# Kernel tuning notes

Hardware: AMD Instinct MI355X
Metric: run time of the kernel (lower is better)

The kernel has to match this reference:

```python
import jax, jax.numpy as jnp
import numpy as np
import math

N_EMBD = 2048
N_HEAD = 16
HEAD_DIM = N_EMBD // N_HEAD
B, T = 2, 2048


def setup_inputs() -> dict:
    key = jax.random.key(0)
    k1, k2, k3 = jax.random.split(key, 3)
    x = jax.random.normal(k1, (B, T, N_EMBD), dtype=jnp.float32)
    # Linear weights stored torch-style [out, in]; applied as x @ W.T
    W_gate = jax.random.normal(k2, (N_HEAD, N_EMBD), dtype=jnp.float32) * 0.02
    W_qkv = jax.random.normal(k3, (3 * N_EMBD, N_EMBD), dtype=jnp.float32) * 0.02
    return {"x": x, "W_gate": W_gate, "W_qkv": W_qkv}


def reference(x, W_gate, W_qkv):
    Bb, Tt, C = x.shape
    H, hd = N_HEAD, HEAD_DIM
    # --- top-1 head gating ---
    gating = jax.nn.softmax(x @ W_gate.T, axis=-1)            # [B,T,H]
    idx = jnp.argmax(gating, axis=-1)                          # [B,T]
    indicator = jax.nn.one_hot(idx, H, dtype=gating.dtype)     # [B,T,H] (no grad, like scatter of ones)
    top1_val = jnp.max(gating, axis=-1, keepdims=True)         # [B,T,1]
    gating_top1 = indicator * top1_val                         # [B,T,H]
    # --- qkv projection ---
    qkv = x @ W_qkv.T                                          # [B,T,3C]
    q, k, v = jnp.split(qkv, 3, axis=-1)
    k = k.reshape(Bb, Tt, H, hd)
    v = v.reshape(Bb, Tt, H, hd)
    # scatter-style weighted collapse of heads -> single shared K/V head (MQA)
    k_shared = jnp.einsum('bth,bthd->btd', indicator, k)       # [B,T,hd]
    v_shared = jnp.einsum('bth,bthd->btd', gating_top1, v)     # [B,T,hd]
    q = q.reshape(Bb, Tt, H, hd).transpose(0, 2, 1, 3)         # [B,H,T,hd]
    # --- causal softmax attention (materialized, as in source) ---
    att = jnp.einsum('bhqd,bkd->bhqk', q, k_shared) * (1.0 / math.sqrt(hd))
    causal = jnp.tril(jnp.ones((Tt, Tt), dtype=bool))          # [T,T]
    att = jnp.where(causal[None, None, :, :], att, -jnp.inf)
    att = jax.nn.softmax(att, axis=-1)
    y = jnp.einsum('bhqk,bkd->bhqd', att, v_shared)            # [B,H,T,hd]
    y = y.transpose(0, 2, 1, 3).reshape(Bb, Tt, C)
    return y
```

## Files before the change

### kernel.cpp

```cpp
#include <hip/hip_runtime.h>
#include <math.h>
#include <cstddef>

#define BB 2
#define TT 2048
#define CC 2048
#define HH 16
#define HD 128
#define MM (BB * TT)
#define QKV_N 6144
#define BK 32

typedef __attribute__((ext_vector_type(8))) short short8;
typedef __attribute__((ext_vector_type(4))) float f32x4;

__device__ __forceinline__ unsigned short f2bf(float f) {
    union { float f; unsigned int u; } v; v.f = f;
    unsigned int r = v.u + 0x7FFFu + ((v.u >> 16) & 1u);
    return (unsigned short)(r >> 16);
}
__device__ __forceinline__ unsigned short f2bf_up(float f) {
    union { float f; unsigned int u; } v; v.f = f;
    return (unsigned short)((v.u + 0x8000u) >> 16);
}
__device__ __forceinline__ float bf2f(unsigned short s) {
    union { unsigned int u; float f; } v; v.u = ((unsigned int)s) << 16;
    return v.f;
}
__device__ __forceinline__ void gload16(const void* g, void* l) {
    __builtin_amdgcn_global_load_lds(
        (const __attribute__((address_space(1))) unsigned int*)g,
        (__attribute__((address_space(3))) unsigned int*)l, 16, 0, 0);
}

__global__ __launch_bounds__(256) void gate_kernel(const float* __restrict__ x,
                                                   const float* __restrict__ Wg,
                                                   int* __restrict__ idxbuf,
                                                   float* __restrict__ top1buf,
                                                   unsigned short* __restrict__ xb) {
    int m = blockIdx.x;
    int tid = threadIdx.x;
    int h = tid >> 4;
    int j = tid & 15;
    const float4* xr = (const float4*)(x + (size_t)m * CC);
    const float4* wr = (const float4*)(Wg + (size_t)h * CC);
    float acc = 0.f;
#pragma unroll 8
    for (int i = 0; i < CC / 4; i += 16) {
        float4 a = xr[i + j];
        float4 b = wr[i + j];
        acc += a.x * b.x + a.y * b.y + a.z * b.z + a.w * b.w;
    }
    for (int off = 8; off > 0; off >>= 1) acc += __shfl_down(acc, off, 16);
    __shared__ float logits[HH];
    if (j == 0) logits[h] = acc;
    {
        float4 a = xr[tid * 2], b = xr[tid * 2 + 1];
        union { unsigned short s[8]; uint4 u; } pk;
        pk.s[0] = f2bf(a.x); pk.s[1] = f2bf(a.y); pk.s[2] = f2bf(a.z); pk.s[3] = f2bf(a.w);
        pk.s[4] = f2bf(b.x); pk.s[5] = f2bf(b.y); pk.s[6] = f2bf(b.z); pk.s[7] = f2bf(b.w);
        ((uint4*)(xb + (size_t)m * CC))[tid] = pk.u;
    }
    __syncthreads();
    if (tid == 0) {
        float zmax = logits[0];
        int best = 0;
        for (int i = 1; i < HH; i++) {
            if (logits[i] > zmax) { zmax = logits[i]; best = i; }
        }
        float s = 0.f;
        for (int i = 0; i < HH; i++) s += expf(logits[i] - zmax);
        idxbuf[m] = best;
        top1buf[m] = 1.0f / s;
    }
}

__global__ __launch_bounds__(256) void convert_bf16(const float* __restrict__ src,
                                                    unsigned short* __restrict__ dst,
                                                    int n8) {
    int i = blockIdx.x * 256 + threadIdx.x;
    if (i >= n8) return;
    const float4* s4 = (const float4*)src;
    float4 a = s4[i * 2], b = s4[i * 2 + 1];
    union { unsigned short s[8]; uint4 u; } pk;
    pk.s[0] = f2bf(a.x); pk.s[1] = f2bf(a.y); pk.s[2] = f2bf(a.z); pk.s[3] = f2bf(a.w);
    pk.s[4] = f2bf(b.x); pk.s[5] = f2bf(b.y); pk.s[6] = f2bf(b.z); pk.s[7] = f2bf(b.w);
    ((uint4*)dst)[i] = pk.u;
}

__global__ __launch_bounds__(256) void qproj_gemm(const unsigned short* __restrict__ A,
                                                  const unsigned short* __restrict__ Bm,
                                                  unsigned short* __restrict__ C) {
    __shared__ unsigned short As[2][128 * BK];
    __shared__ unsigned short Bs[2][128 * BK];
    int tid = threadIdx.x;
    int wave = tid >> 6, lane = tid & 63;
    int l = lane & 15, g = lane >> 4;
    int m0 = blockIdx.y * 128, n0 = blockIdx.x * 128;
    int wr = wave >> 1, wc = wave & 1;

    f32x4 acc[4][4];
#pragma unroll
    for (int i = 0; i < 4; i++)
#pragma unroll
        for (int j = 0; j < 4; j++) acc[i][j] = (f32x4){0.f, 0.f, 0.f, 0.f};

    int srow = lane >> 2;
    int scol = (lane & 3) * 8;
    const unsigned short* aB0 = A + (size_t)(m0 + wave * 32 + srow) * 2048 + scol;
    const unsigned short* bB0 = Bm + (size_t)(n0 + wave * 32 + srow) * 2048 + scol;

#define QSTAGE(k0_, bi) do {                                                   \
        gload16(aB0 + (k0_), &As[bi][wave * 1024]);                            \
        gload16(aB0 + (k0_) + (size_t)16 * 2048, &As[bi][wave * 1024 + 512]);  \
        gload16(bB0 + (k0_), &Bs[bi][wave * 1024]);                            \
        gload16(bB0 + (k0_) + (size_t)16 * 2048, &Bs[bi][wave * 1024 + 512]);  \
    } while (0)

    QSTAGE(0, 0);
    __syncthreads();

    for (int k0 = 0; k0 < 2048; k0 += BK) {
        int cur = (k0 >> 5) & 1;
        if (k0 + BK < 2048) QSTAGE(k0 + BK, cur ^ 1);
        short8 af[4], bf[4];
#pragma unroll
        for (int i = 0; i < 4; i++)
            af[i] = *(const short8*)&As[cur][(wr * 64 + i * 16 + l) * BK + g * 8];
#pragma unroll
        for (int j = 0; j < 4; j++)
            bf[j] = *(const short8*)&Bs[cur][(wc * 64 + j * 16 + l) * BK + g * 8];
#pragma unroll
        for (int i = 0; i < 4; i++)
#pragma unroll
            for (int j = 0; j < 4; j++)
                acc[i][j] = __builtin_amdgcn_mfma_f32_16x16x32_bf16(af[i], bf[j], acc[i][j], 0, 0, 0);
        __syncthreads();
    }
#undef QSTAGE

    const float qscale = 0.08838834764831845f;
#pragma unroll
    for (int j = 0; j < 4; j++) {
        int col = n0 + wc * 64 + j * 16 + l;
#pragma unroll
        for (int i = 0; i < 4; i++) {
            int row = m0 + wr * 64 + i * 16 + g * 4;
#pragma unroll
            for (int r = 0; r < 4; r++)
                C[(size_t)(row + r) * CC + col] = f2bf(acc[i][j][r] * qscale);
        }
    }
}

__global__ __launch_bounds__(256) void bucket_kernel(const int* __restrict__ idxb,
                                                     int* __restrict__ ord,
                                                     int* __restrict__ hs) {
    __shared__ unsigned short cnts[256][16];
    __shared__ int hsum[16], hbase[16];
    int t = threadIdx.x;
    unsigned short c[16];
#pragma unroll
    for (int h = 0; h < 16; h++) c[h] = 0;
    int hv[16];
#pragma unroll
    for (int i = 0; i < 16; i++) {
        hv[i] = idxb[t * 16 + i];
        c[hv[i]]++;
    }
#pragma unroll
    for (int h = 0; h < 16; h++) cnts[t][h] = c[h];
    __syncthreads();
    if (t < 16) {
        int s = 0;
        for (int j = 0; j < 256; j++) {
            int v = cnts[j][t];
            cnts[j][t] = (unsigned short)s;
            s += v;
        }
        hsum[t] = s;
    }
    __syncthreads();
    if (t == 0) {
        int s = 0;
        for (int h = 0; h < 16; h++) { hbase[h] = s; hs[h] = s; s += hsum[h]; }
        hs[16] = s;
    }
    __syncthreads();
    int pos[16];
#pragma unroll
    for (int h = 0; h < 16; h++) pos[h] = hbase[h] + (int)cnts[t][h];
#pragma unroll
    for (int i = 0; i < 16; i++) {
        int h = hv[i];
        ord[pos[h]++] = t * 16 + i;
    }
}

__global__ __launch_bounds__(256) void kvsel_gemm(const unsigned short* __restrict__ xb,
                                                  const unsigned short* __restrict__ wb,
                                                  const int* __restrict__ ord,
                                                  const int* __restrict__ hs,
                                                  const float* __restrict__ top1,
                                                  unsigned short* __restrict__ kshB,
                                                  unsigned short* __restrict__ vshT) {
    __shared__ unsigned short As[2][64 * 32];
    __shared__ unsigned short Bs[2][128 * 32];
    int h = blockIdx.x, reg = blockIdx.y, mt = blockIdx.z;
    int s0 = hs[h], s1 = hs[h + 1];
    int cnt = s1 - s0;
    if (mt * 64 >= cnt) return;
    int base = s0 + mt * 64;
    int tid = threadIdx.x;
    int wave = tid >> 6, lane = tid & 63;
    int l = lane & 15, g = lane >> 4;

    int arow = base + wave * 16 + (lane >> 2);
    int atok = ord[(arow < s1) ? arow : (s1 - 1)];
    const unsigned short* aSrc = xb + (size_t)atok * CC + (lane & 3) * 8;
    int wr0 = 2048 + reg * 2048 + h * 128;
    const unsigned short* bSrc0 = wb + (size_t)(wr0 + (wave * 2 + 0) * 16 + (lane >> 2)) * CC + (lane & 3) * 8;
    const unsigned short* bSrc1 = wb + (size_t)(wr0 + (wave * 2 + 1) * 16 + (lane >> 2)) * CC + (lane & 3) * 8;

#define KSTAGE(k0_, bi) do {                                    \
        gload16(aSrc + (k0_), &As[bi][wave * 512]);             \
        gload16(bSrc0 + (k0_), &Bs[bi][(wave * 2 + 0) * 512]);  \
        gload16(bSrc1 + (k0_), &Bs[bi][(wave * 2 + 1) * 512]);  \
    } while (0)

    f32x4 acc[8];
#pragma unroll
    for (int j = 0; j < 8; j++) acc[j] = (f32x4){0.f, 0.f, 0.f, 0.f};

    KSTAGE(0, 0);
    __syncthreads();

    for (int k0 = 0; k0 < 2048; k0 += 32) {
        int cur = (k0 >> 5) & 1;
        if (k0 + 32 < 2048) KSTAGE(k0 + 32, cur ^ 1);
        short8 af = *(const short8*)&As[cur][(wave * 16 + l) * 32 + g * 8];
#pragma unroll
        for (int j = 0; j < 8; j++) {
            short8 bf = *(const short8*)&Bs[cur][(j * 16 + l) * 32 + g * 8];
            acc[j] = __builtin_amdgcn_mfma_f32_16x16x32_bf16(af, bf, acc[j], 0, 0, 0);
        }
        __syncthreads();
    }
#undef KSTAGE

#pragma unroll
    for (int i = 0; i < 4; i++) {
        int r = wave * 16 + g * 4 + i;
        if (base + r >= s1) continue;
        int tok = ord[base + r];
        if (reg == 0) {
#pragma unroll
            for (int j = 0; j < 8; j++)
                kshB[(size_t)tok * HD + j * 16 + l] = f2bf(acc[j][i]);
        } else {
            float tv = top1[tok];
#pragma unroll
            for (int j = 0; j < 8; j++)
                vshT[(size_t)(j * 16 + l) * MM + tok] = f2bf(acc[j][i] * tv);
        }
    }
}

__global__ __launch_bounds__(256) void attn_mfma(const unsigned short* __restrict__ qb,
                                                 const unsigned short* __restrict__ kb,
                                                 const unsigned short* __restrict__ vtb,
                                                 float* __restrict__ y) {
    __shared__ unsigned short KsA[2][32 * 128];
    __shared__ unsigned short VtA[2][128 * 32];
    __shared__ unsigned short Ps[4][2][16][40];

    int bid = blockIdx.x;
    int ql = 64 + (bid >> 3);
    int b  = (bid >> 2) & 1;
    int hq = bid & 3;
    int qs = 127 - ql;
    int q0l = ql * 16, q0s = qs * 16;
    int nchL = (ql >> 1) + 1;
    int nchS = (qs >> 1) + 1;
    int tid = threadIdx.x;
    int wave = tid >> 6;
    int lane = tid & 63;
    int l = lane & 15;
    int g = lane >> 4;
    int h = hq * 4 + wave;

    short8 qf[2][4];
#pragma unroll
    for (int qt = 0; qt < 2; qt++) {
        int q0 = qt ? q0s : q0l;
        const unsigned short* qrow = qb + (size_t)(b * TT + q0 + l) * CC + h * HD;
#pragma unroll
        for (int kc = 0; kc < 4; kc++)
            qf[qt][kc] = *(const short8*)(qrow + kc * 32 + g * 8);
    }

    short8 onesf;
    {
        short v = (l == 0) ? (short)0x3F80 : (short)0;
#pragma unroll
        for (int e = 0; e < 8; e++) onesf[e] = v;
    }

    f32x4 o[2][8];
    f32x4 o8[2];
#pragma unroll
    for (int qt = 0; qt < 2; qt++) {
#pragma unroll
        for (int n = 0; n < 8; n++) o[qt][n] = (f32x4){0.f, 0.f, 0.f, 0.f};
        o8[qt] = (f32x4){0.f, 0.f, 0.f, 0.f};
    }

    const unsigned short* kbase = kb + (size_t)b * TT * HD;
    int rbaseL = q0l + g * 4;
    int rbaseS = q0s + g * 4;

#define STAGE(cc, bufi) do {                                                      \
        int kc0_ = (cc) * 32;                                                     \
        _Pragma("unroll")                                                         \
        for (int rep_ = 0; rep_ < 2; rep_++) {                                    \
            int s_ = tid + rep_ * 256;                                            \
            int kr_ = s_ >> 4, kp_ = s_ & 15;                                     \
            gload16(kbase + (size_t)(kc0_ + kr_) * HD + ((kp_ ^ (kr_ & 15)) * 8), \
                    &KsA[bufi][(rep_ * 256 + wave * 64) * 8]);                    \
            int vd_ = s_ >> 2, vp_ = s_ & 3;                                      \
            int vq_ = vp_ ^ ((vd_ >> 1) & 3);                                     \
            gload16(vtb + (size_t)vd_ * MM + b * TT + kc0_ + vq_ * 8,             \
                    &VtA[bufi][(rep_ * 256 + wave * 64) * 8]);                    \
        }                                                                         \
    } while (0)

    STAGE(0, 0);
    __syncthreads();

    for (int c = 0; c < nchL; c++) {
        int kc0 = c * 32;
        int cur = c & 1;
        if (c + 1 < nchL) STAGE(c + 1, cur ^ 1);
        bool sAct = (c < nchS);
        bool diagL = (c == nchL - 1);
        bool diagS = (c == nchS - 1);
        const unsigned short* Kc = KsA[cur];
        const unsigned short* Vc = VtA[cur];

#pragma unroll
        for (int t = 0; t < 2; t++) {
            short8 kf[4];
#pragma unroll
            for (int kc = 0; kc < 4; kc++)
                kf[kc] = *(const short8*)&Kc[(t * 16 + l) * 128 + (((kc * 4 + g) ^ l) * 8)];
            f32x4 sl = (f32x4){0.f, 0.f, 0.f, 0.f};
#pragma unroll
            for (int kc = 0; kc < 4; kc++)
                sl = __builtin_amdgcn_mfma_f32_16x16x32_bf16(qf[0][kc], kf[kc], sl, 0, 0, 0);
            if (diagL) {
                int key = kc0 + t * 16 + l;
#pragma unroll
                for (int i = 0; i < 4; i++)
                    if (key > rbaseL + i) sl[i] = -1e30f;
            }
#pragma unroll
            for (int i = 0; i < 4; i++)
                Ps[wave][0][g * 4 + i][t * 16 + l] = f2bf_up(__expf(sl[i] - 30.f));
            if (sAct) {
                f32x4 ss = (f32x4){0.f, 0.f, 0.f, 0.f};
#pragma unroll
                for (int kc = 0; kc < 4; kc++)
                    ss = __builtin_amdgcn_mfma_f32_16x16x32_bf16(qf[1][kc], kf[kc], ss, 0, 0, 0);
                if (diagS) {
                    int key = kc0 + t * 16 + l;
#pragma unroll
                    for (int i = 0; i < 4; i++)
                        if (key > rbaseS + i) ss[i] = -1e30f;
                }
#pragma unroll
                for (int i = 0; i < 4; i++)
                    Ps[wave][1][g * 4 + i][t * 16 + l] = f2bf_up(__expf(ss[i] - 30.f));
            }
        }
        {
            short8 pf0 = *(const short8*)&Ps[wave][0][l][g * 8];
            if (sAct) {
                short8 pf1 = *(const short8*)&Ps[wave][1][l][g * 8];
#pragma unroll
                for (int n = 0; n < 8; n++) {
                    short8 vf = *(const short8*)&Vc[(n * 16 + l) * 32 + ((g ^ ((l >> 1) & 3)) * 8)];
                    o[0][n] = __builtin_amdgcn_mfma_f32_16x16x32_bf16(pf0, vf, o[0][n], 0, 0, 0);
                    o[1][n] = __builtin_amdgcn_mfma_f32_16x16x32_bf16(pf1, vf, o[1][n], 0, 0, 0);
                }
                o8[0] = __builtin_amdgcn_mfma_f32_16x16x32_bf16(pf0, onesf, o8[0], 0, 0, 0);
                o8[1] = __builtin_amdgcn_mfma_f32_16x16x32_bf16(pf1, onesf, o8[1], 0, 0, 0);
            } else {
#pragma unroll
                for (int n = 0; n < 8; n++) {
                    short8 vf = *(const short8*)&Vc[(n * 16 + l) * 32 + ((g ^ ((l >> 1) & 3)) * 8)];
                    o[0][n] = __builtin_amdgcn_mfma_f32_16x16x32_bf16(pf0, vf, o[0][n], 0, 0, 0);
                }
                o8[0] = __builtin_amdgcn_mfma_f32_16x16x32_bf16(pf0, onesf, o8[0], 0, 0, 0);
            }
        }
        __syncthreads();
    }
#undef STAGE

#pragma unroll
    for (int qt = 0; qt < 2; qt++) {
        int q0 = qt ? q0s : q0l;
        float inv[4];
#pragma unroll
        for (int i = 0; i < 4; i++) {
            float lv = __shfl(o8[qt][i], lane & 48);
            inv[i] = 1.f / lv;
        }
#pragma unroll
        for (int n = 0; n < 8; n++) {
#pragma unroll
            for (int i = 0; i < 4; i++) {
                y[(size_t)(b * TT + q0 + g * 4 + i) * CC + h * HD + n * 16 + l] =
                    o[qt][n][i] * inv[i];
            }
        }
    }
}

extern "C" void kernel_launch(void* const* d_in, const int* in_sizes, int n_in,
                              void* d_out, int out_size, void* d_ws, size_t ws_size,
                              hipStream_t stream) {
    (void)in_sizes; (void)n_in; (void)out_size; (void)ws_size;
    const float* x    = (const float*)d_in[0];
    const float* Wg   = (const float*)d_in[1];
    const float* Wqkv = (const float*)d_in[2];
    float* y = (float*)d_out;

    unsigned short* xb   = (unsigned short*)d_ws;
    unsigned short* wb   = xb + (size_t)MM * CC;
    unsigned short* qbuf = wb + (size_t)QKV_N * CC;
    unsigned short* kshB = qbuf + (size_t)MM * CC;
    unsigned short* vshT = kshB + (size_t)MM * HD;
    float* top1 = (float*)(vshT + (size_t)HD * MM);
    int*   idxb = (int*)(top1 + MM);
    int*   ord  = idxb + MM;
    int*   hs   = ord + MM;

    gate_kernel<<<MM, 256, 0, stream>>>(x, Wg, idxb, top1, xb);
    convert_bf16<<<(QKV_N * CC / 8 + 255) / 256, 256, 0, stream>>>(Wqkv, wb, QKV_N * CC / 8);
    qproj_gemm<<<dim3(16, 32), 256, 0, stream>>>(xb, wb, qbuf);
    bucket_kernel<<<1, 256, 0, stream>>>(idxb, ord, hs);
    kvsel_gemm<<<dim3(16, 2, 64), 256, 0, stream>>>(xb, wb, ord, hs, top1, kshB, vshT);
    attn_mfma<<<512, 256, 0, stream>>>(qbuf, kshB, vshT, y);
}
```

Measured before the change: 333.5 us.

## Split paired long/short query tiles into separate blocks with snake ordering

The attention kernel previously paired a long and a short causal query tile in one block so the K/V chunk loads were shared and per-block work was balanced. The change gives each block a single 16-row query tile, doubling the grid to 1024 blocks. Blocks are ordered longest-first, with every second group of 256 reversed so that heavy and light tiles are spread across CUs. It also halves the accumulator and Q register footprint and adds a launch bound of 4 blocks per CU to raise occupancy. The cost is that K/V tiles are now loaded twice as often from global memory, and scheduling balance depends on how the hardware dispatches blocks.

New measurement: 309.3 us. 7.3% less time.

```diff
diff --git a/kernel.cpp b/kernel.cpp
--- a/kernel.cpp
+++ b/kernel.cpp
@@ -266,22 +266,22 @@
     }
 }
 
-__global__ __launch_bounds__(256) void attn_mfma(const unsigned short* __restrict__ qb,
-                                                 const unsigned short* __restrict__ kb,
-                                                 const unsigned short* __restrict__ vtb,
-                                                 float* __restrict__ y) {
+__global__ __launch_bounds__(256, 4) void attn_mfma(const unsigned short* __restrict__ qb,
+                                                    const unsigned short* __restrict__ kb,
+                                                    const unsigned short* __restrict__ vtb,
+                                                    float* __restrict__ y) {
     __shared__ unsigned short KsA[2][32 * 128];
     __shared__ unsigned short VtA[2][128 * 32];
-    __shared__ unsigned short Ps[4][2][16][40];
+    __shared__ unsigned short Ps[4][16][40];
 
     int bid = blockIdx.x;
-    int ql = 64 + (bid >> 3);
-    int b  = (bid >> 2) & 1;
-    int hq = bid & 3;
-    int qs = 127 - ql;
-    int q0l = ql * 16, q0s = qs * 16;
-    int nchL = (ql >> 1) + 1;
-    int nchS = (qs >> 1) + 1;
+    int t = bid & 255, r = bid >> 8;
+    int k = (r << 8) | ((r & 1) ? (255 - t) : t);
+    int qi = 127 - (k >> 3);
+    int b  = (k >> 2) & 1;
+    int hq = k & 3;
+    int q0 = qi * 16;
+    int nch = (qi >> 1) + 1;
     int tid = threadIdx.x;
     int wave = tid >> 6;
     int lane = tid & 63;
@@ -289,14 +289,12 @@
     int g = lane >> 4;
     int h = hq * 4 + wave;
 
-    short8 qf[2][4];
-#pragma unroll
-    for (int qt = 0; qt < 2; qt++) {
-        int q0 = qt ? q0s : q0l;
+    short8 qf[4];
+    {
         const unsigned short* qrow = qb + (size_t)(b * TT + q0 + l) * CC + h * HD;
 #pragma unroll
         for (int kc = 0; kc < 4; kc++)
-            qf[qt][kc] = *(const short8*)(qrow + kc * 32 + g * 8);
+            qf[kc] = *(const short8*)(qrow + kc * 32 + g * 8);
     }
 
     short8 onesf;
@@ -306,18 +304,13 @@
         for (int e = 0; e < 8; e++) onesf[e] = v;
     }
 
-    f32x4 o[2][8];
-    f32x4 o8[2];
-#pragma unroll
-    for (int qt = 0; qt < 2; qt++) {
-#pragma unroll
-        for (int n = 0; n < 8; n++) o[qt][n] = (f32x4){0.f, 0.f, 0.f, 0.f};
-        o8[qt] = (f32x4){0.f, 0.f, 0.f, 0.f};
-    }
+    f32x4 o[8];
+    f32x4 o8 = (f32x4){0.f, 0.f, 0.f, 0.f};
+#pragma unroll
+    for (int n = 0; n < 8; n++) o[n] = (f32x4){0.f, 0.f, 0.f, 0.f};
 
     const unsigned short* kbase = kb + (size_t)b * TT * HD;
-    int rbaseL = q0l + g * 4;
-    int rbaseS = q0s + g * 4;
+    int rbase = q0 + g * 4;
 
 #define STAGE(cc, bufi) do {                                                      \
         int kc0_ = (cc) * 32;                                                     \
@@ -337,83 +330,52 @@
     STAGE(0, 0);
     __syncthreads();
 
-    for (int c = 0; c < nchL; c++) {
+    for (int c = 0; c < nch; c++) {
         int kc0 = c * 32;
         int cur = c & 1;
-        if (c + 1 < nchL) STAGE(c + 1, cur ^ 1);
-        bool sAct = (c < nchS);
-        bool diagL = (c == nchL - 1);
-        bool diagS = (c == nchS - 1);
+        if (c + 1 < nch) STAGE(c + 1, cur ^ 1);
+        bool diag = (c == nch - 1);
         const unsigned short* Kc = KsA[cur];
         const unsigned short* Vc = VtA[cur];
 
 #pragma unroll
-        for (int t = 0; t < 2; t++) {
+        for (int tt = 0; tt < 2; tt++) {
             short8 kf[4];
 #pragma unroll
             for (int kc = 0; kc < 4; kc++)
-                kf[kc] = *(const short8*)&Kc[(t * 16 + l) * 128 + (((kc * 4 + g) ^ l) * 8)];
+                kf[kc] = *(const short8*)&Kc[(tt * 16 + l) * 128 + (((kc * 4 + g) ^ l) * 8)];
             f32x4 sl = (f32x4){0.f, 0.f, 0.f, 0.f};
 #pragma unroll
             for (int kc = 0; kc < 4; kc++)
-                sl = __builtin_amdgcn_mfma_f32_16x16x32_bf16(qf[0][kc], kf[kc], sl, 0, 0, 0);
-            if (diagL) {
-                int key = kc0 + t * 16 + l;
+                sl = __builtin_amdgcn_mfma_f32_16x16x32_bf16(qf[kc], kf[kc], sl, 0, 0, 0);
+            if (diag) {
+                int key = kc0 + tt * 16 + l;
 #pragma unroll
                 for (int i = 0; i < 4; i++)
-                    if (key > rbaseL + i) sl[i] = -1e30f;
+                    if (key > rbase + i) sl[i] = -1e30f;
             }
 #pragma unroll
             for (int i = 0; i < 4; i++)
-                Ps[wave][0][g * 4 + i][t * 16 + l] = f2bf_up(__expf(sl[i] - 30.f));
-            if (sAct) {
-                f32x4 ss = (f32x4){0.f, 0.f, 0.f, 0.f};
-#pragma unroll
-                for (int kc = 0; kc < 4; kc++)
-                    ss = __builtin_amdgcn_mfma_f32_16x16x32_bf16(qf[1][kc], kf[kc], ss, 0, 0, 0);
-                if (diagS) {
-                    int key = kc0 + t * 16 + l;
-#pragma unroll
-                    for (int i = 0; i < 4; i++)
-                        if (key > rbaseS + i) ss[i] = -1e30f;
-                }
-#pragma unroll
-                for (int i = 0; i < 4; i++)
-                    Ps[wave][1][g * 4 + i][t * 16 + l] = f2bf_up(__expf(ss[i] - 30.f));
+                Ps[wave][g * 4 + i][tt * 16 + l] = f2bf_up(__expf(sl[i] - 30.f));
+        }
+        {
+            short8 pf0 = *(const short8*)&Ps[wave][l][g * 8];
+#pragma unroll
+            for (int n = 0; n < 8; n++) {
+                short8 vf = *(const short8*)&Vc[(n * 16 + l) * 32 + ((g ^ ((l >> 1) & 3)) * 8)];
+                o[n] = __builtin_amdgcn_mfma_f32_16x16x32_bf16(pf0, vf, o[n], 0, 0, 0);
             }
-        }
-        {
-            short8 pf0 = *(const short8*)&Ps[wave][0][l][g * 8];
-            if (sAct) {
-                short8 pf1 = *(const short8*)&Ps[wave][1][l][g * 8];
-#pragma unroll
-                for (int n = 0; n < 8; n++) {
-                    short8 vf = *(const short8*)&Vc[(n * 16 + l) * 32 + ((g ^ ((l >> 1) & 3)) * 8)];
-                    o[0][n] = __builtin_amdgcn_mfma_f32_16x16x32_bf16(pf0, vf, o[0][n], 0, 0, 0);
-                    o[1][n] = __builtin_amdgcn_mfma_f32_16x16x32_bf16(pf1, vf, o[1][n], 0, 0, 0);
-                }
-                o8[0] = __builtin_amdgcn_mfma_f32_16x16x32_bf16(pf0, onesf, o8[0], 0, 0, 0);
-                o8[1] = __builtin_amdgcn_mfma_f32_16x16x32_bf16(pf1, onesf, o8[1], 0, 0, 0);
-            } else {
-#pragma unroll
-                for (int n = 0; n < 8; n++) {
-                    short8 vf = *(const short8*)&Vc[(n * 16 + l) * 32 + ((g ^ ((l >> 1) & 3)) * 8)];
-                    o[0][n] = __builtin_amdgcn_mfma_f32_16x16x32_bf16(pf0, vf, o[0][n], 0, 0, 0);
-                }
-                o8[0] = __builtin_amdgcn_mfma_f32_16x16x32_bf16(pf0, onesf, o8[0], 0, 0, 0);
-            }
+            o8 = __builtin_amdgcn_mfma_f32_16x16x32_bf16(pf0, onesf, o8, 0, 0, 0);
         }
         __syncthreads();
     }
 #undef STAGE
 
-#pragma unroll
-    for (int qt = 0; qt < 2; qt++) {
-        int q0 = qt ? q0s : q0l;
+    {
         float inv[4];
 #pragma unroll
         for (int i = 0; i < 4; i++) {
-            float lv = __shfl(o8[qt][i], lane & 48);
+            float lv = __shfl(o8[i], lane & 48);
             inv[i] = 1.f / lv;
         }
 #pragma unroll
@@ -421,7 +383,7 @@
 #pragma unroll
             for (int i = 0; i < 4; i++) {
                 y[(size_t)(b * TT + q0 + g * 4 + i) * CC + h * HD + n * 16 + l] =
-                    o[qt][n][i] * inv[i];
+                    o[n][i] * inv[i];
             }
         }
     }
@@ -451,5 +413,5 @@
     qproj_gemm<<<dim3(16, 32), 256, 0, stream>>>(xb, wb, qbuf);
     bucket_kernel<<<1, 256, 0, stream>>>(idxb, ord, hs);
     kvsel_gemm<<<dim3(16, 2, 64), 256, 0, stream>>>(xb, wb, ord, hs, top1, kshB, vshT);
-    attn_mfma<<<512, 256, 0, stream>>>(qbuf, kshB, vshT, y);
-}
+    attn_mfma<<<1024, 256, 0, stream>>>(qbuf, kshB, vshT, y);
+}
```
